# Optimization experiments

Hardware: AMD Instinct MI355X
Metric: run time of the kernel (lower is better)

The kernel has to match this reference:

```python
import jax, jax.numpy as jnp
import numpy as np

N = 131072
N_SIGMAS = 64
SEG = N // N_SIGMAS  # 2048, also the gaussian window size


def setup_inputs() -> dict:
    key = jax.random.key(0)
    ks = jax.random.split(key, 4)
    n, h = 256, 256
    x = jax.random.normal(ks[0], (n,), dtype=jnp.float32)
    W1 = jax.random.normal(ks[1], (n, h), dtype=jnp.float32) / jnp.sqrt(jnp.float32(n))
    b1 = jnp.zeros((h,), dtype=jnp.float32)
    W2 = jax.random.normal(ks[2], (h, N_SIGMAS), dtype=jnp.float32) / jnp.sqrt(jnp.float32(h))
    b2 = jnp.zeros((N_SIGMAS,), dtype=jnp.float32)
    W3 = jax.random.normal(ks[3], (n, N), dtype=jnp.float32) / jnp.sqrt(jnp.float32(n))
    b3 = jnp.zeros((N,), dtype=jnp.float32)
    return {"x": x, "W1": W1, "b1": b1, "W2": W2, "b2": b2, "W3": W3, "b3": b3}


def _gaussian_windows(sigmas):
    # gaussian_kernel(window_size=SEG, sigma) vmapped over sigmas -> (n_sigmas, SEG)
    mu = SEG / 2.0
    t = jnp.arange(SEG, dtype=sigmas.dtype)
    w = jnp.exp(-((t[None, :] - mu) ** 2) / (2.0 * sigmas[:, None] ** 2))
    return w / jnp.sum(w, axis=1, keepdims=True)


def reference(x, W1, b1, W2, b2, W3, b3):
    # sigma-predictor MLP: Dense -> swish -> Dense
    s = jax.nn.swish(jnp.dot(x, W1) + b1)
    sigmas = jnp.dot(s, W2) + b2              # (n_sigmas,)
    y = jnp.dot(x, W3) + b3                   # (N,)
    windows = _gaussian_windows(sigmas)       # (n_sigmas, SEG)
    segs = y.reshape(N_SIGMAS, SEG)           # equal split, N divisible by n_sigmas
    out = jax.vmap(lambda a, w: jnp.convolve(a, w, mode="same"))(segs, windows)
    return out.reshape(-1)                    # hstack of segments
```

## Files before the change

kernel.cpp:

```cpp
#include <hip/hip_runtime.h>
#include <math.h>

#define NTOT 131072
#define NSIG 64
#define SEGL 2048
#define NIN 256


__global__ __launch_bounds__(256) void k_y(
    const float* __restrict__ x,  const float* __restrict__ W1,
    const float* __restrict__ b1, const float* __restrict__ W2,
    const float* __restrict__ b2, const float* __restrict__ W3,
    const float* __restrict__ b3, float* __restrict__ y,
    float* __restrict__ w_all, int* __restrict__ Dv)
{
  __shared__ float xl[NIN];
  __shared__ float sl[256];
  __shared__ float red[4];
  __shared__ float bc[2];

  const int t = threadIdx.x;
  const int bx0 = (int)blockIdx.x;
  const int bx = ((bx0 & 7) << 6) | (bx0 >> 3);
  const int col = (bx << 8) + t;

  xl[t] = x[t];
  __syncthreads();

  const float* p = W3 + col;
  float a = b3[col];

  if (bx0 < NSIG) {
    float am = b1[t];
    #pragma unroll 32
    for (int n = 0; n < NIN; ++n) {
      const float xv = xl[n];
      a  = fmaf(xv, p[(size_t)n * NTOT], a);
      am = fmaf(xv, W1[n * 256 + t], am);
    }
    y[col] = a;
    sl[t] = am / (1.0f + expf(-am));
    __syncthreads();

    const int seg = bx0;
    float v = sl[t] * W2[t * NSIG + seg];
    #pragma unroll
    for (int o = 32; o > 0; o >>= 1) v += __shfl_down(v, o, 64);
    const int lane = t & 63, wid = t >> 6;
    if (lane == 0) red[wid] = v;
    __syncthreads();
    if (t == 0) bc[0] = red[0] + red[1] + red[2] + red[3] + b2[seg];
    __syncthreads();
    const float sig = bc[0];

    const float inv2 = 1.0f / (2.0f * sig * sig);
    const float Df = 12.0f * fabsf(sig) + 4.0f;
    const int D = (Df >= 1024.0f) ? 1024 : (int)Df;
    const int dlo = -D;
    const int dhi = (D < 1023) ? D : 1023;
    const int cnt = dhi - dlo + 1;

    float zp = 0.0f;
    for (int i = t; i < cnt; i += 256) {
      const float d = (float)(dlo + i);
      const float e = expf(-d * d * inv2);
      w_all[seg * SEGL + 1024 + dlo + i] = e;
      zp += e;
    }
    v = zp;
    #pragma unroll
    for (int o = 32; o > 0; o >>= 1) v += __shfl_down(v, o, 64);
    if (lane == 0) red[wid] = v;
    __syncthreads();
    if (t == 0) bc[1] = red[0] + red[1] + red[2] + red[3];
    __syncthreads();
    const float iZ = 1.0f / bc[1];
    for (int i = t; i < cnt; i += 256)
      w_all[seg * SEGL + 1024 + dlo + i] *= iZ;
    if (t == 0) Dv[seg] = D;
  } else {
    #pragma unroll 32
    for (int n = 0; n < NIN; ++n)
      a = fmaf(xl[n], p[(size_t)n * NTOT], a);
    y[col] = a;
  }
}

__global__ __launch_bounds__(256) void k_conv(
    const float* __restrict__ y, const float* __restrict__ w_all,
    const int* __restrict__ Dv, float* __restrict__ out)
{
  __shared__ float S[2560];

  const int t = threadIdx.x;
  const int bx0 = (int)blockIdx.x;
  const int bx = ((bx0 & 7) << 6) | (bx0 >> 3);
  const int seg = bx >> 3;
  const int M0 = (bx & 7) << 8;
  const int sbase = M0 - 1026;

  const int D = Dv[seg];
  const int dlo = -D;
  const int dhi = (D < 1023) ? D : 1023;

  const int ilo = 1025 - dhi;
  const int ihi = 1281 + D;
  for (int i = ilo + t; i < ihi; i += 256) {
    const int g = sbase + i;
    S[i] = (g >= 0 && g < SEGL) ? y[seg * SEGL + g] : 0.0f;
  }
  __syncthreads();

  const float* wrow = w_all + seg * SEGL + 1024;
  float a = 0.0f;
  for (int d = dlo; d <= dhi; ++d)
    a = fmaf(wrow[d], S[t + 1025 - d], a);
  out[seg * SEGL + M0 + t] = a;
}

extern "C" void kernel_launch(void* const* d_in, const int* in_sizes, int n_in,
                              void* d_out, int out_size, void* d_ws, size_t ws_size,
                              hipStream_t stream) {
  const float* x  = (const float*)d_in[0];
  const float* W1 = (const float*)d_in[1];
  const float* b1 = (const float*)d_in[2];
  const float* W2 = (const float*)d_in[3];
  const float* b2 = (const float*)d_in[4];
  const float* W3 = (const float*)d_in[5];
  const float* b3 = (const float*)d_in[6];
  float* out = (float*)d_out;

  char* ws = (char*)d_ws;
  float* y     = (float*)(ws);
  float* w_all = (float*)(ws + 524288);
  int*   Dv    = (int*)  (ws + 1048576);

  hipLaunchKernelGGL(k_y, dim3(512), dim3(256), 0, stream,
                     x, W1, b1, W2, b2, W3, b3, y, w_all, Dv);
  hipLaunchKernelGGL(k_conv, dim3(512), dim3(256), 0, stream,
                     y, w_all, Dv, out);
}
```

Before: 31.91 us.

## Split the W3 GEMV reduction across two blocks and sum the halves in the convolution load

The x·W3 GEMV is now split along the reduction dimension into two 128-row halves, which doubles the grid to 1024 blocks and gives more parallelism and memory-level concurrency for streaming the 128 MB W3. Each half writes a partial y to the workspace. The convolution kernel adds the two partials plus b3 when it stages the segment into shared memory. The sigma-predictor MLP is decoupled from the W3 loop and runs after it in the first 64 blocks. This costs an extra partial-vector write and read, plus a larger workspace.

```diff
diff --git a/kernel.cpp b/kernel.cpp
--- a/kernel.cpp
+++ b/kernel.cpp
@@ -11,8 +11,7 @@
     const float* __restrict__ x,  const float* __restrict__ W1,
     const float* __restrict__ b1, const float* __restrict__ W2,
     const float* __restrict__ b2, const float* __restrict__ W3,
-    const float* __restrict__ b3, float* __restrict__ y,
-    float* __restrict__ w_all, int* __restrict__ Dv)
+    float* __restrict__ y01, float* __restrict__ w_all, int* __restrict__ Dv)
 {
   __shared__ float xl[NIN];
   __shared__ float sl[256];
@@ -21,74 +20,71 @@
 
   const int t = threadIdx.x;
   const int bx0 = (int)blockIdx.x;
-  const int bx = ((bx0 & 7) << 6) | (bx0 >> 3);
-  const int col = (bx << 8) + t;
+  const int bx = ((bx0 & 7) << 7) | (bx0 >> 3);
+  const int chunk = bx >> 1;
+  const int half = bx & 1;
+  const int col = (chunk << 8) + t;
 
   xl[t] = x[t];
   __syncthreads();
 
-  const float* p = W3 + col;
-  float a = b3[col];
+  const float* p = W3 + (size_t)(half << 7) * NTOT + col;
+  float a = 0.0f;
+  #pragma unroll 16
+  for (int k = 0; k < 128; ++k)
+    a = fmaf(xl[(half << 7) + k], p[(size_t)k * NTOT], a);
+  y01[half * NTOT + col] = a;
 
-  if (bx0 < NSIG) {
-    float am = b1[t];
-    #pragma unroll 32
-    for (int n = 0; n < NIN; ++n) {
-      const float xv = xl[n];
-      a  = fmaf(xv, p[(size_t)n * NTOT], a);
-      am = fmaf(xv, W1[n * 256 + t], am);
-    }
-    y[col] = a;
-    sl[t] = am / (1.0f + expf(-am));
-    __syncthreads();
+  if (bx0 >= NSIG) return;
 
-    const int seg = bx0;
-    float v = sl[t] * W2[t * NSIG + seg];
-    #pragma unroll
-    for (int o = 32; o > 0; o >>= 1) v += __shfl_down(v, o, 64);
-    const int lane = t & 63, wid = t >> 6;
-    if (lane == 0) red[wid] = v;
-    __syncthreads();
-    if (t == 0) bc[0] = red[0] + red[1] + red[2] + red[3] + b2[seg];
-    __syncthreads();
-    const float sig = bc[0];
+  const int seg = bx0;
+  float am = b1[t];
+  #pragma unroll 16
+  for (int n = 0; n < NIN; ++n) am = fmaf(xl[n], W1[n * 256 + t], am);
+  sl[t] = am / (1.0f + expf(-am));
+  __syncthreads();
 
-    const float inv2 = 1.0f / (2.0f * sig * sig);
-    const float Df = 12.0f * fabsf(sig) + 4.0f;
-    const int D = (Df >= 1024.0f) ? 1024 : (int)Df;
-    const int dlo = -D;
-    const int dhi = (D < 1023) ? D : 1023;
-    const int cnt = dhi - dlo + 1;
+  float v = sl[t] * W2[t * NSIG + seg];
+  #pragma unroll
+  for (int o = 32; o > 0; o >>= 1) v += __shfl_down(v, o, 64);
+  const int lane = t & 63, wid = t >> 6;
+  if (lane == 0) red[wid] = v;
+  __syncthreads();
+  if (t == 0) bc[0] = red[0] + red[1] + red[2] + red[3] + b2[seg];
+  __syncthreads();
+  const float sig = bc[0];
 
-    float zp = 0.0f;
-    for (int i = t; i < cnt; i += 256) {
-      const float d = (float)(dlo + i);
-      const float e = expf(-d * d * inv2);
-      w_all[seg * SEGL + 1024 + dlo + i] = e;
-      zp += e;
-    }
-    v = zp;
-    #pragma unroll
-    for (int o = 32; o > 0; o >>= 1) v += __shfl_down(v, o, 64);
-    if (lane == 0) red[wid] = v;
-    __syncthreads();
-    if (t == 0) bc[1] = red[0] + red[1] + red[2] + red[3];
-    __syncthreads();
-    const float iZ = 1.0f / bc[1];
-    for (int i = t; i < cnt; i += 256)
-      w_all[seg * SEGL + 1024 + dlo + i] *= iZ;
-    if (t == 0) Dv[seg] = D;
-  } else {
-    #pragma unroll 32
-    for (int n = 0; n < NIN; ++n)
-      a = fmaf(xl[n], p[(size_t)n * NTOT], a);
-    y[col] = a;
+  const float inv2 = 1.0f / (2.0f * sig * sig);
+  const float Df = 12.0f * fabsf(sig) + 4.0f;
+  const int D = (Df >= 1024.0f) ? 1024 : (int)Df;
+  const int dlo = -D;
+  const int dhi = (D < 1023) ? D : 1023;
+  const int cnt = dhi - dlo + 1;
+
+  float zp = 0.0f;
+  for (int i = t; i < cnt; i += 256) {
+    const float d = (float)(dlo + i);
+    const float e = expf(-d * d * inv2);
+    w_all[seg * SEGL + 1024 + dlo + i] = e;
+    zp += e;
   }
+  v = zp;
+  #pragma unroll
+  for (int o = 32; o > 0; o >>= 1) v += __shfl_down(v, o, 64);
+  if (lane == 0) red[wid] = v;
+  __syncthreads();
+  if (t == 0) bc[1] = red[0] + red[1] + red[2] + red[3];
+  __syncthreads();
+  const float iZ = 1.0f / bc[1];
+  for (int i = t; i < cnt; i += 256)
+    w_all[seg * SEGL + 1024 + dlo + i] *= iZ;
+  if (t == 0) Dv[seg] = D;
 }
 
 __global__ __launch_bounds__(256) void k_conv(
-    const float* __restrict__ y, const float* __restrict__ w_all,
-    const int* __restrict__ Dv, float* __restrict__ out)
+    const float* __restrict__ y01, const float* __restrict__ b3,
+    const float* __restrict__ w_all, const int* __restrict__ Dv,
+    float* __restrict__ out)
 {
   __shared__ float S[2560];
 
@@ -107,7 +103,12 @@
   const int ihi = 1281 + D;
   for (int i = ilo + t; i < ihi; i += 256) {
     const int g = sbase + i;
-    S[i] = (g >= 0 && g < SEGL) ? y[seg * SEGL + g] : 0.0f;
+    float v = 0.0f;
+    if (g >= 0 && g < SEGL) {
+      const int idx = seg * SEGL + g;
+      v = y01[idx] + y01[NTOT + idx] + b3[idx];
+    }
+    S[i] = v;
   }
   __syncthreads();
 
@@ -131,12 +132,12 @@
   float* out = (float*)d_out;
 
   char* ws = (char*)d_ws;
-  float* y     = (float*)(ws);
-  float* w_all = (float*)(ws + 524288);
-  int*   Dv    = (int*)  (ws + 1048576);
+  float* y01   = (float*)(ws);
+  float* w_all = (float*)(ws + 1048576);
+  int*   Dv    = (int*)  (ws + 1572864);
 
-  hipLaunchKernelGGL(k_y, dim3(512), dim3(256), 0, stream,
-                     x, W1, b1, W2, b2, W3, b3, y, w_all, Dv);
+  hipLaunchKernelGGL(k_y, dim3(1024), dim3(256), 0, stream,
+                     x, W1, b1, W2, b2, W3, y01, w_all, Dv);
   hipLaunchKernelGGL(k_conv, dim3(512), dim3(256), 0, stream,
-                     y, w_all, Dv, out);
+                     y01, b3, w_all, Dv, out);
 }
```

Result: slower. 34.67 us (+8.7%).
